# Kernel tuning notes

Hardware: AMD Instinct MI355X
Metric: run time of the kernel (lower is better)

Reference implementation:

```python
import jax, jax.numpy as jnp
import numpy as np

N_NODES = 500_000
MEM_DIM = 256
MSG_DIM = 256
N_UPD = 100_000


def setup_inputs() -> dict:
    key = jax.random.key(0)
    ks = jax.random.split(key, 10)
    s = 1.0 / np.sqrt(MEM_DIM)
    return {
        "unique_node_ids": jnp.arange(N_UPD, dtype=jnp.int64)
        if jax.config.jax_enable_x64 else jnp.arange(N_UPD, dtype=jnp.int32),
        "unique_messages": jax.random.normal(ks[0], (N_UPD, MSG_DIM), jnp.float32),
        "timestamps": jax.random.uniform(ks[1], (N_UPD,), jnp.float32),
        "net_transaction_amounts": jax.random.normal(ks[2], (N_UPD,), jnp.float32),
        "memory": jax.random.normal(ks[3], (N_NODES, MEM_DIM), jnp.float32),
        "last_update": jnp.zeros((N_NODES,), jnp.float32),
        "W_cat": jax.random.normal(ks[4], (MEM_DIM, MSG_DIM + 1), jnp.float32) * s,
        "b_cat": jnp.zeros((MEM_DIM,), jnp.float32),
        "W_ih": jax.random.normal(ks[5], (3 * MEM_DIM, MEM_DIM), jnp.float32) * s,
        "W_hh": jax.random.normal(ks[6], (3 * MEM_DIM, MEM_DIM), jnp.float32) * s,
        "b_ih": jnp.zeros((3 * MEM_DIM,), jnp.float32),
        "b_hh": jnp.zeros((3 * MEM_DIM,), jnp.float32),
    }


def _gru_cell(x, h, W_ih, W_hh, b_ih, b_hh):
    # torch.nn.GRUCell math
    gi = x @ W_ih.T + b_ih      # [N, 3*D]
    gh = h @ W_hh.T + b_hh      # [N, 3*D]
    i_r, i_z, i_n = jnp.split(gi, 3, axis=1)
    h_r, h_z, h_n = jnp.split(gh, 3, axis=1)
    r = jax.nn.sigmoid(i_r + h_r)
    z = jax.nn.sigmoid(i_z + h_z)
    n = jnp.tanh(i_n + r * h_n)
    return (1.0 - z) * n + z * h


def reference(unique_node_ids, unique_messages, timestamps, net_transaction_amounts,
              memory, last_update, W_cat, b_cat, W_ih, W_hh, b_ih, b_hh):
    # concat message with scalar amount, small linear projection
    cat = jnp.concatenate([unique_messages, net_transaction_amounts[:, None]], axis=1)
    final_inputs = cat @ W_cat.T + b_cat                # [N_upd, MEM_DIM]
    h = memory[unique_node_ids]                         # gather by id
    new_h = _gru_cell(final_inputs, h, W_ih, W_hh, b_ih, b_hh)
    updated_memory = memory.at[unique_node_ids].set(new_h)        # scatter back
    updated_last_update = last_update.at[unique_node_ids].set(timestamps)
    return updated_memory, updated_last_update
```

## Files before the change

kernel.cpp:

```cpp
#include <hip/hip_runtime.h>
#include <hip/hip_bf16.h>

typedef __attribute__((ext_vector_type(8))) short s16x8;
typedef __attribute__((ext_vector_type(4))) float f32x4;

__device__ __forceinline__ unsigned short f2bf(float x) {
    unsigned int u = __float_as_uint(x);
    u += 0x7fffu + ((u >> 16) & 1u);
    return (unsigned short)(u >> 16);
}
__device__ __forceinline__ float bf2f(unsigned short h) {
    return __uint_as_float((unsigned int)h << 16);
}
__device__ __forceinline__ s16x8 pack8(float4 a, float4 b) {
    return (s16x8){ (short)f2bf(a.x), (short)f2bf(a.y), (short)f2bf(a.z), (short)f2bf(a.w),
                    (short)f2bf(b.x), (short)f2bf(b.y), (short)f2bf(b.z), (short)f2bf(b.w) };
}
__device__ __forceinline__ void gload_lds16(const void* g, void* l) {
    __builtin_amdgcn_global_load_lds(
        (const __attribute__((address_space(1))) void*)g,
        (__attribute__((address_space(3))) void*)(unsigned int)(size_t)l,
        16, 0, 0);
}
__device__ __forceinline__ float sigf(float x) { return 1.f / (1.f + __expf(-x)); }
__device__ __forceinline__ float tanhfast(float x) {
    return 1.f - 2.f / (__expf(2.f * x) + 1.f);
}

__global__ void prep_w_kernel(const float* __restrict__ W_cat,
                              const float* __restrict__ b_cat,
                              const float* __restrict__ W_ih,
                              const float* __restrict__ W_hh,
                              const float* __restrict__ b_ih,
                              const int* __restrict__ ids,
                              unsigned short* __restrict__ wm,
                              unsigned short* __restrict__ whh,
                              float* __restrict__ wamt,
                              float* __restrict__ bcomb,
                              int* __restrict__ inv,
                              int M) {
    int idx = blockIdx.x * blockDim.x + threadIdx.x;
    const int NW = 768 * 256;
    if (idx < NW) {
        int g = idx >> 8, c = idx & 255;
        float s = 0.f;
        #pragma unroll 4
        for (int k = 0; k < 256; ++k) s += W_ih[g * 256 + k] * W_cat[k * 257 + c];
        wm[idx] = f2bf(s);
    } else if (idx < 2 * NW) {
        int t = idx - NW;
        whh[t] = f2bf(W_hh[t]);
    } else if (idx < 2 * NW + 768) {
        int g = idx - 2 * NW;
        float sa = 0.f, sb = 0.f;
        for (int k = 0; k < 256; ++k) {
            float w = W_ih[g * 256 + k];
            sa += w * W_cat[k * 257 + 256];
            sb += w * b_cat[k];
        }
        wamt[g] = sa;
        bcomb[g] = sb + b_ih[g];
    } else if (idx < 2 * NW + 768 + M) {
        int i = idx - (2 * NW + 768);
        inv[ids[i]] = i + 1;
    }
}

__device__ __forceinline__ void dma_w(const unsigned short* __restrict__ wm,
                                      const unsigned short* __restrict__ whh,
                                      int nc, int k0, char* swbuf, int tid) {
    #pragma unroll
    for (int it = 0; it < 6; ++it) {
        int q = tid + it * 512;
        int r = q >> 3;
        int part = (q & 7) ^ (r & 7);
        int pn = r >> 6, rr = r & 63;
        const unsigned short* src = (pn < 3)
            ? wm  + ((size_t)(pn * 256 + nc * 64 + rr)) * 256
            : whh + ((size_t)((pn - 3) * 256 + nc * 64 + rr)) * 256;
        gload_lds16((const char*)src + k0 * 2 + part * 16,
                    swbuf + (tid & ~63) * 16 + it * 8192);
    }
}

__global__ __launch_bounds__(512, 2)
void gru_kernel(const int* __restrict__ ids,
                const float* __restrict__ msgs,
                const float* __restrict__ memory,
                const unsigned short* __restrict__ wm,
                const unsigned short* __restrict__ whh,
                const float* __restrict__ wamt,
                const float* __restrict__ bcomb,
                const float* __restrict__ b_hh,
                const float* __restrict__ amt,
                float* __restrict__ out_mem,
                int M, int mtiles) {
    extern __shared__ char lds[];
    char* sm  = lds;
    char* sh  = lds + 16384;
    char* sw0 = lds + 32768;
    char* sw1 = lds + 81920;

    int g = blockIdx.x;
    int xcd = g & 7, s = g >> 3;
    int nc = s & 3;
    int mtile = (s >> 2) * 8 + xcd;
    if (mtile >= mtiles) return;
    int m0 = mtile * 128;

    int tid = threadIdx.x;
    int lane = tid & 63;
    int w = tid >> 6;
    int wr = w >> 2, wc = w & 3;

    int row0 = tid >> 3, row1 = (tid + 512) >> 3;
    int part = tid & 7;
    int gr0 = m0 + row0; if (gr0 >= M) gr0 = M - 1;
    int gr1 = m0 + row1; if (gr1 >= M) gr1 = M - 1;
    const float* mp0 = msgs + (size_t)gr0 * 256 + part * 8;
    const float* mp1 = msgs + (size_t)gr1 * 256 + part * 8;
    const float* hp0 = memory + (size_t)ids[gr0] * 256 + part * 8;
    const float* hp1 = memory + (size_t)ids[gr1] * 256 + part * 8;
    int ld0 = row0 * 128 + ((part ^ (row0 & 7)) * 16);
    int ld1 = row1 * 128 + ((part ^ (row1 & 7)) * 16);

    float4 ma0, mb0, ma1, mb1, ha0, hb0, ha1, hb1;
    {
        int k0 = ((nc + 1) & 3) * 64;
        ma0 = *(const float4*)(mp0 + k0);  mb0 = *(const float4*)(mp0 + k0 + 4);
        ma1 = *(const float4*)(mp1 + k0);  mb1 = *(const float4*)(mp1 + k0 + 4);
        ha0 = *(const float4*)(hp0 + k0);  hb0 = *(const float4*)(hp0 + k0 + 4);
        ha1 = *(const float4*)(hp1 + k0);  hb1 = *(const float4*)(hp1 + k0 + 4);
        dma_w(wm, whh, nc, k0, sw0, tid);
        *(s16x8*)(sm + ld0) = pack8(ma0, mb0);
        *(s16x8*)(sm + ld1) = pack8(ma1, mb1);
        *(s16x8*)(sh + ld0) = pack8(ha0, hb0);
        *(s16x8*)(sh + ld1) = pack8(ha1, hb1);
    }
    __syncthreads();

    f32x4 acc[6][4];
    #pragma unroll
    for (int pn = 0; pn < 6; ++pn)
        #pragma unroll
        for (int mf = 0; mf < 4; ++mf) acc[pn][mf] = (f32x4){0.f, 0.f, 0.f, 0.f};

    #pragma unroll
    for (int ks = 0; ks < 4; ++ks) {
        char* swc = (ks & 1) ? sw1 : sw0;
        if (ks < 3) {
            int k0 = ((nc + 2 + ks) & 3) * 64;
            ma0 = *(const float4*)(mp0 + k0);  mb0 = *(const float4*)(mp0 + k0 + 4);
            ma1 = *(const float4*)(mp1 + k0);  mb1 = *(const float4*)(mp1 + k0 + 4);
            ha0 = *(const float4*)(hp0 + k0);  hb0 = *(const float4*)(hp0 + k0 + 4);
            ha1 = *(const float4*)(hp1 + k0);  hb1 = *(const float4*)(hp1 + k0 + 4);
            dma_w(wm, whh, nc, k0, (ks & 1) ? sw0 : sw1, tid);
        }
        #pragma unroll
        for (int c = 0; c < 2; ++c) {
            int p = c * 4 + (lane >> 4);
            s16x8 ax[4], ah[4], bw[6];
            #pragma unroll
            for (int mf = 0; mf < 4; ++mf) {
                int row = wr * 64 + mf * 16 + (lane & 15);
                int off = row * 128 + ((p ^ (row & 7)) * 16);
                ax[mf] = *(const s16x8*)(sm + off);
                ah[mf] = *(const s16x8*)(sh + off);
            }
            #pragma unroll
            for (int pn = 0; pn < 6; ++pn) {
                int r = pn * 64 + wc * 16 + (lane & 15);
                bw[pn] = *(const s16x8*)(swc + r * 128 + ((p ^ (r & 7)) * 16));
            }
            #pragma unroll
            for (int pn = 0; pn < 6; ++pn)
                #pragma unroll
                for (int mf = 0; mf < 4; ++mf)
                    acc[pn][mf] = __builtin_amdgcn_mfma_f32_16x16x32_bf16(
                        (pn < 3) ? ax[mf] : ah[mf], bw[pn], acc[pn][mf], 0, 0, 0);
        }
        if (ks < 3) {
            __syncthreads();
            *(s16x8*)(sm + ld0) = pack8(ma0, mb0);
            *(s16x8*)(sm + ld1) = pack8(ma1, mb1);
            *(s16x8*)(sh + ld0) = pack8(ha0, hb0);
            *(s16x8*)(sh + ld1) = pack8(ha1, hb1);
            __syncthreads();
        }
    }

    int colL = wc * 16 + (lane & 15);
    int col = nc * 64 + colL;
    float bi0 = bcomb[col], bi1 = bcomb[256 + col], bi2 = bcomb[512 + col];
    float bh0 = b_hh[col],  bh1 = b_hh[256 + col],  bh2 = b_hh[512 + col];
    float wa0 = wamt[col],  wa1 = wamt[256 + col],  wa2 = wamt[512 + col];
    int hpart = colL >> 3, hbyte = (colL & 7) << 1;
    #pragma unroll
    for (int mf = 0; mf < 4; ++mf) {
        int rb = wr * 64 + mf * 16 + (lane >> 4) * 4;
        #pragma unroll
        for (int r = 0; r < 4; ++r) {
            int rl = rb + r;
            int grow = m0 + rl; if (grow >= M) grow = M - 1;
            int gid = ids[grow];
            float amtv = amt[grow];
            float hv = bf2f(*(const unsigned short*)(
                sh + rl * 128 + ((hpart ^ (rl & 7)) << 4) + hbyte));
            float ir = acc[0][mf][r] + bi0 + amtv * wa0;
            float iz = acc[1][mf][r] + bi1 + amtv * wa1;
            float in_ = acc[2][mf][r] + bi2 + amtv * wa2;
            float hr = acc[3][mf][r] + bh0;
            float hz = acc[4][mf][r] + bh1;
            float hn = acc[5][mf][r] + bh2;
            float rg = sigf(ir + hr);
            float zg = sigf(iz + hz);
            float ng = tanhfast(in_ + rg * hn);
            out_mem[(size_t)gid * 256 + col] = (1.f - zg) * ng + zg * hv;
        }
    }
}

__global__ __launch_bounds__(256)
void copy_kernel(const float* __restrict__ memory,
                 const int* __restrict__ inv,
                 const float* __restrict__ lu,
                 const float* __restrict__ ts,
                 float* __restrict__ out_mem,
                 float* __restrict__ out_lu,
                 int N) {
    int wid = (blockIdx.x * blockDim.x + threadIdx.x) >> 6;
    int lane = threadIdx.x & 63;
    int nw = (gridDim.x * blockDim.x) >> 6;
    for (int base = wid; base < N; base += nw * 4) {
        int  r0 = base, r1 = base + nw, r2 = base + 2 * nw, r3 = base + 3 * nw;
        bool d0 = (r0 < N) && (inv[r0] == 0);
        bool d1 = (r1 < N) && (inv[r1] == 0);
        bool d2 = (r2 < N) && (inv[r2] == 0);
        bool d3 = (r3 < N) && (inv[r3] == 0);
        float4 v0, v1, v2, v3;
        if (d0) v0 = ((const float4*)(memory + (size_t)r0 * 256))[lane];
        if (d1) v1 = ((const float4*)(memory + (size_t)r1 * 256))[lane];
        if (d2) v2 = ((const float4*)(memory + (size_t)r2 * 256))[lane];
        if (d3) v3 = ((const float4*)(memory + (size_t)r3 * 256))[lane];
        if (d0) ((float4*)(out_mem + (size_t)r0 * 256))[lane] = v0;
        if (d1) ((float4*)(out_mem + (size_t)r1 * 256))[lane] = v1;
        if (d2) ((float4*)(out_mem + (size_t)r2 * 256))[lane] = v2;
        if (d3) ((float4*)(out_mem + (size_t)r3 * 256))[lane] = v3;
    }
    int gidx = blockIdx.x * blockDim.x + threadIdx.x;
    int stride = gridDim.x * blockDim.x;
    for (int i = gidx; i < N; i += stride) {
        int iv = inv[i];
        out_lu[i] = iv ? ts[iv - 1] : lu[i];
    }
}

extern "C" void kernel_launch(void* const* d_in, const int* in_sizes, int n_in,
                              void* d_out, int out_size, void* d_ws, size_t ws_size,
                              hipStream_t stream) {
    const int*   ids   = (const int*)  d_in[0];
    const float* msgs  = (const float*)d_in[1];
    const float* ts    = (const float*)d_in[2];
    const float* amt   = (const float*)d_in[3];
    const float* mem   = (const float*)d_in[4];
    const float* lu    = (const float*)d_in[5];
    const float* W_cat = (const float*)d_in[6];
    const float* b_cat = (const float*)d_in[7];
    const float* W_ih  = (const float*)d_in[8];
    const float* W_hh  = (const float*)d_in[9];
    const float* b_ih  = (const float*)d_in[10];
    const float* b_hh  = (const float*)d_in[11];

    int M = in_sizes[0];
    int N = in_sizes[5];

    float* out_mem = (float*)d_out;
    float* out_lu  = out_mem + (size_t)N * 256;

    char* ws = (char*)d_ws;
    unsigned short* wm    = (unsigned short*)ws;
    unsigned short* whh   = wm + 768 * 256;
    float*          wamt  = (float*)(whh + 768 * 256);
    float*          bcomb = wamt + 768;
    int*            inv   = (int*)(bcomb + 768);

    (void)hipMemsetAsync(inv, 0, (size_t)N * 4, stream);

    int prep_items = 2 * 768 * 256 + 768 + M;
    prep_w_kernel<<<(prep_items + 255) / 256, 256, 0, stream>>>(
        W_cat, b_cat, W_ih, W_hh, b_ih, ids, wm, whh, wamt, bcomb, inv, M);

    int mtiles = (M + 127) / 128;
    int mt8 = ((mtiles + 7) / 8) * 8;
    (void)hipFuncSetAttribute((const void*)gru_kernel,
                              hipFuncAttributeMaxDynamicSharedMemorySize, 131072);
    gru_kernel<<<mt8 * 4, 512, 131072, stream>>>(
        ids, msgs, mem, wm, whh, wamt, bcomb, b_hh, amt, out_mem, M, mtiles);

    copy_kernel<<<2048, 256, 0, stream>>>(mem, inv, lu, ts, out_mem, out_lu, N);
}
```

Measured before the change: 396.7 us.

## Shrink GRU tiles to 64 rows, single-buffer weights, fold memset and lu scatter

```diff
diff --git a/kernel.cpp b/kernel.cpp
--- a/kernel.cpp
+++ b/kernel.cpp
@@ -38,7 +38,7 @@
                               float* __restrict__ wamt,
                               float* __restrict__ bcomb,
                               int* __restrict__ inv,
-                              int M) {
+                              int N, int M) {
     int idx = blockIdx.x * blockDim.x + threadIdx.x;
     const int NW = 768 * 256;
     if (idx < NW) {
@@ -60,163 +60,11 @@
         }
         wamt[g] = sa;
         bcomb[g] = sb + b_ih[g];
-    } else if (idx < 2 * NW + 768 + M) {
-        int i = idx - (2 * NW + 768);
+    } else if (idx < 2 * NW + 768 + N) {
+        inv[idx - (2 * NW + 768)] = 0;
+    } else if (idx < 2 * NW + 768 + N + M) {
+        int i = idx - (2 * NW + 768 + N);
         inv[ids[i]] = i + 1;
-    }
-}
-
-__device__ __forceinline__ void dma_w(const unsigned short* __restrict__ wm,
-                                      const unsigned short* __restrict__ whh,
-                                      int nc, int k0, char* swbuf, int tid) {
-    #pragma unroll
-    for (int it = 0; it < 6; ++it) {
-        int q = tid + it * 512;
-        int r = q >> 3;
-        int part = (q & 7) ^ (r & 7);
-        int pn = r >> 6, rr = r & 63;
-        const unsigned short* src = (pn < 3)
-            ? wm  + ((size_t)(pn * 256 + nc * 64 + rr)) * 256
-            : whh + ((size_t)((pn - 3) * 256 + nc * 64 + rr)) * 256;
-        gload_lds16((const char*)src + k0 * 2 + part * 16,
-                    swbuf + (tid & ~63) * 16 + it * 8192);
-    }
-}
-
-__global__ __launch_bounds__(512, 2)
-void gru_kernel(const int* __restrict__ ids,
-                const float* __restrict__ msgs,
-                const float* __restrict__ memory,
-                const unsigned short* __restrict__ wm,
-                const unsigned short* __restrict__ whh,
-                const float* __restrict__ wamt,
-                const float* __restrict__ bcomb,
-                const float* __restrict__ b_hh,
-                const float* __restrict__ amt,
-                float* __restrict__ out_mem,
-                int M, int mtiles) {
-    extern __shared__ char lds[];
-    char* sm  = lds;
-    char* sh  = lds + 16384;
-    char* sw0 = lds + 32768;
-    char* sw1 = lds + 81920;
-
-    int g = blockIdx.x;
-    int xcd = g & 7, s = g >> 3;
-    int nc = s & 3;
-    int mtile = (s >> 2) * 8 + xcd;
-    if (mtile >= mtiles) return;
-    int m0 = mtile * 128;
-
-    int tid = threadIdx.x;
-    int lane = tid & 63;
-    int w = tid >> 6;
-    int wr = w >> 2, wc = w & 3;
-
-    int row0 = tid >> 3, row1 = (tid + 512) >> 3;
-    int part = tid & 7;
-    int gr0 = m0 + row0; if (gr0 >= M) gr0 = M - 1;
-    int gr1 = m0 + row1; if (gr1 >= M) gr1 = M - 1;
-    const float* mp0 = msgs + (size_t)gr0 * 256 + part * 8;
-    const float* mp1 = msgs + (size_t)gr1 * 256 + part * 8;
-    const float* hp0 = memory + (size_t)ids[gr0] * 256 + part * 8;
-    const float* hp1 = memory + (size_t)ids[gr1] * 256 + part * 8;
-    int ld0 = row0 * 128 + ((part ^ (row0 & 7)) * 16);
-    int ld1 = row1 * 128 + ((part ^ (row1 & 7)) * 16);
-
-    float4 ma0, mb0, ma1, mb1, ha0, hb0, ha1, hb1;
-    {
-        int k0 = ((nc + 1) & 3) * 64;
-        ma0 = *(const float4*)(mp0 + k0);  mb0 = *(const float4*)(mp0 + k0 + 4);
-        ma1 = *(const float4*)(mp1 + k0);  mb1 = *(const float4*)(mp1 + k0 + 4);
-        ha0 = *(const float4*)(hp0 + k0);  hb0 = *(const float4*)(hp0 + k0 + 4);
-        ha1 = *(const float4*)(hp1 + k0);  hb1 = *(const float4*)(hp1 + k0 + 4);
-        dma_w(wm, whh, nc, k0, sw0, tid);
-        *(s16x8*)(sm + ld0) = pack8(ma0, mb0);
-        *(s16x8*)(sm + ld1) = pack8(ma1, mb1);
-        *(s16x8*)(sh + ld0) = pack8(ha0, hb0);
-        *(s16x8*)(sh + ld1) = pack8(ha1, hb1);
-    }
-    __syncthreads();
-
-    f32x4 acc[6][4];
-    #pragma unroll
-    for (int pn = 0; pn < 6; ++pn)
-        #pragma unroll
-        for (int mf = 0; mf < 4; ++mf) acc[pn][mf] = (f32x4){0.f, 0.f, 0.f, 0.f};
-
-    #pragma unroll
-    for (int ks = 0; ks < 4; ++ks) {
-        char* swc = (ks & 1) ? sw1 : sw0;
-        if (ks < 3) {
-            int k0 = ((nc + 2 + ks) & 3) * 64;
-            ma0 = *(const float4*)(mp0 + k0);  mb0 = *(const float4*)(mp0 + k0 + 4);
-            ma1 = *(const float4*)(mp1 + k0);  mb1 = *(const float4*)(mp1 + k0 + 4);
-            ha0 = *(const float4*)(hp0 + k0);  hb0 = *(const float4*)(hp0 + k0 + 4);
-            ha1 = *(const float4*)(hp1 + k0);  hb1 = *(const float4*)(hp1 + k0 + 4);
-            dma_w(wm, whh, nc, k0, (ks & 1) ? sw0 : sw1, tid);
-        }
-        #pragma unroll
-        for (int c = 0; c < 2; ++c) {
-            int p = c * 4 + (lane >> 4);
-            s16x8 ax[4], ah[4], bw[6];
-            #pragma unroll
-            for (int mf = 0; mf < 4; ++mf) {
-                int row = wr * 64 + mf * 16 + (lane & 15);
-                int off = row * 128 + ((p ^ (row & 7)) * 16);
-                ax[mf] = *(const s16x8*)(sm + off);
-                ah[mf] = *(const s16x8*)(sh + off);
-            }
-            #pragma unroll
-            for (int pn = 0; pn < 6; ++pn) {
-                int r = pn * 64 + wc * 16 + (lane & 15);
-                bw[pn] = *(const s16x8*)(swc + r * 128 + ((p ^ (r & 7)) * 16));
-            }
-            #pragma unroll
-            for (int pn = 0; pn < 6; ++pn)
-                #pragma unroll
-                for (int mf = 0; mf < 4; ++mf)
-                    acc[pn][mf] = __builtin_amdgcn_mfma_f32_16x16x32_bf16(
-                        (pn < 3) ? ax[mf] : ah[mf], bw[pn], acc[pn][mf], 0, 0, 0);
-        }
-        if (ks < 3) {
-            __syncthreads();
-            *(s16x8*)(sm + ld0) = pack8(ma0, mb0);
-            *(s16x8*)(sm + ld1) = pack8(ma1, mb1);
-            *(s16x8*)(sh + ld0) = pack8(ha0, hb0);
-            *(s16x8*)(sh + ld1) = pack8(ha1, hb1);
-            __syncthreads();
-        }
-    }
-
-    int colL = wc * 16 + (lane & 15);
-    int col = nc * 64 + colL;
-    float bi0 = bcomb[col], bi1 = bcomb[256 + col], bi2 = bcomb[512 + col];
-    float bh0 = b_hh[col],  bh1 = b_hh[256 + col],  bh2 = b_hh[512 + col];
-    float wa0 = wamt[col],  wa1 = wamt[256 + col],  wa2 = wamt[512 + col];
-    int hpart = colL >> 3, hbyte = (colL & 7) << 1;
-    #pragma unroll
-    for (int mf = 0; mf < 4; ++mf) {
-        int rb = wr * 64 + mf * 16 + (lane >> 4) * 4;
-        #pragma unroll
-        for (int r = 0; r < 4; ++r) {
-            int rl = rb + r;
-            int grow = m0 + rl; if (grow >= M) grow = M - 1;
-            int gid = ids[grow];
-            float amtv = amt[grow];
-            float hv = bf2f(*(const unsigned short*)(
-                sh + rl * 128 + ((hpart ^ (rl & 7)) << 4) + hbyte));
-            float ir = acc[0][mf][r] + bi0 + amtv * wa0;
-            float iz = acc[1][mf][r] + bi1 + amtv * wa1;
-            float in_ = acc[2][mf][r] + bi2 + amtv * wa2;
-            float hr = acc[3][mf][r] + bh0;
-            float hz = acc[4][mf][r] + bh1;
-            float hn = acc[5][mf][r] + bh2;
-            float rg = sigf(ir + hr);
-            float zg = sigf(iz + hz);
-            float ng = tanhfast(in_ + rg * hn);
-            out_mem[(size_t)gid * 256 + col] = (1.f - zg) * ng + zg * hv;
-        }
     }
 }
 
@@ -224,7 +72,6 @@
 void copy_kernel(const float* __restrict__ memory,
                  const int* __restrict__ inv,
                  const float* __restrict__ lu,
-                 const float* __restrict__ ts,
                  float* __restrict__ out_mem,
                  float* __restrict__ out_lu,
                  int N) {
@@ -249,9 +96,165 @@
     }
     int gidx = blockIdx.x * blockDim.x + threadIdx.x;
     int stride = gridDim.x * blockDim.x;
-    for (int i = gidx; i < N; i += stride) {
-        int iv = inv[i];
-        out_lu[i] = iv ? ts[iv - 1] : lu[i];
+    for (int i = gidx; i < N; i += stride) out_lu[i] = lu[i];
+}
+
+__device__ __forceinline__ void dma_w(const unsigned short* __restrict__ wm,
+                                      const unsigned short* __restrict__ whh,
+                                      int nc, int k0, char* swbuf, int tid) {
+    #pragma unroll
+    for (int it = 0; it < 12; ++it) {
+        int q = tid + it * 256;
+        int r = q >> 3;
+        int part = (q & 7) ^ (r & 7);
+        int pn = r >> 6, rr = r & 63;
+        const unsigned short* src = (pn < 3)
+            ? wm  + ((size_t)(pn * 256 + nc * 64 + rr)) * 256
+            : whh + ((size_t)((pn - 3) * 256 + nc * 64 + rr)) * 256;
+        gload_lds16((const char*)src + k0 * 2 + part * 16,
+                    swbuf + (q & ~63) * 16);
+    }
+}
+
+__global__ __launch_bounds__(256, 2)
+void gru_kernel(const int* __restrict__ ids,
+                const float* __restrict__ msgs,
+                const float* __restrict__ memory,
+                const unsigned short* __restrict__ wm,
+                const unsigned short* __restrict__ whh,
+                const float* __restrict__ wamt,
+                const float* __restrict__ bcomb,
+                const float* __restrict__ b_hh,
+                const float* __restrict__ amt,
+                const float* __restrict__ ts,
+                float* __restrict__ out_mem,
+                float* __restrict__ out_lu,
+                int M, int mtiles) {
+    extern __shared__ char lds[];
+    char* sm = lds;
+    char* sh = lds + 8192;
+    char* sw = lds + 16384;
+
+    int g = blockIdx.x;
+    int xcd = g & 7, s = g >> 3;
+    int nc = s & 3;
+    int mtile = (s >> 2) * 8 + xcd;
+    if (mtile >= mtiles) return;
+    int m0 = mtile * 64;
+
+    int tid = threadIdx.x;
+    int lane = tid & 63;
+    int wc = tid >> 6;
+
+    int row0 = tid >> 3, row1 = (tid + 256) >> 3;
+    int part = tid & 7;
+    int gr0 = m0 + row0; if (gr0 >= M) gr0 = M - 1;
+    int gr1 = m0 + row1; if (gr1 >= M) gr1 = M - 1;
+    const float* mp0 = msgs + (size_t)gr0 * 256 + part * 8;
+    const float* mp1 = msgs + (size_t)gr1 * 256 + part * 8;
+    const float* hp0 = memory + (size_t)ids[gr0] * 256 + part * 8;
+    const float* hp1 = memory + (size_t)ids[gr1] * 256 + part * 8;
+    int ld0 = row0 * 128 + ((part ^ (row0 & 7)) * 16);
+    int ld1 = row1 * 128 + ((part ^ (row1 & 7)) * 16);
+
+    s16x8 pm0, pm1, ph0, ph1;
+    {
+        int k0 = ((nc + 1) & 3) * 64;
+        float4 a0 = *(const float4*)(mp0 + k0), b0 = *(const float4*)(mp0 + k0 + 4);
+        float4 a1 = *(const float4*)(mp1 + k0), b1 = *(const float4*)(mp1 + k0 + 4);
+        float4 c0 = *(const float4*)(hp0 + k0), d0 = *(const float4*)(hp0 + k0 + 4);
+        float4 c1 = *(const float4*)(hp1 + k0), d1 = *(const float4*)(hp1 + k0 + 4);
+        dma_w(wm, whh, nc, k0, sw, tid);
+        *(s16x8*)(sm + ld0) = pack8(a0, b0);
+        *(s16x8*)(sm + ld1) = pack8(a1, b1);
+        *(s16x8*)(sh + ld0) = pack8(c0, d0);
+        *(s16x8*)(sh + ld1) = pack8(c1, d1);
+    }
+    __syncthreads();
+
+    f32x4 acc[6][4];
+    #pragma unroll
+    for (int pn = 0; pn < 6; ++pn)
+        #pragma unroll
+        for (int mf = 0; mf < 4; ++mf) acc[pn][mf] = (f32x4){0.f, 0.f, 0.f, 0.f};
+
+    #pragma unroll
+    for (int ks = 0; ks < 4; ++ks) {
+        float4 a0, b0, a1, b1, c0, d0, c1, d1;
+        if (ks < 3) {
+            int k0 = ((nc + 2 + ks) & 3) * 64;
+            a0 = *(const float4*)(mp0 + k0);  b0 = *(const float4*)(mp0 + k0 + 4);
+            a1 = *(const float4*)(mp1 + k0);  b1 = *(const float4*)(mp1 + k0 + 4);
+            c0 = *(const float4*)(hp0 + k0);  d0 = *(const float4*)(hp0 + k0 + 4);
+            c1 = *(const float4*)(hp1 + k0);  d1 = *(const float4*)(hp1 + k0 + 4);
+        }
+        #pragma unroll
+        for (int c = 0; c < 2; ++c) {
+            int p = c * 4 + (lane >> 4);
+            s16x8 ax[4], ah[4], bw[6];
+            #pragma unroll
+            for (int mf = 0; mf < 4; ++mf) {
+                int row = mf * 16 + (lane & 15);
+                int off = row * 128 + ((p ^ (row & 7)) * 16);
+                ax[mf] = *(const s16x8*)(sm + off);
+                ah[mf] = *(const s16x8*)(sh + off);
+            }
+            #pragma unroll
+            for (int pn = 0; pn < 6; ++pn) {
+                int r = pn * 64 + wc * 16 + (lane & 15);
+                bw[pn] = *(const s16x8*)(sw + r * 128 + ((p ^ (r & 7)) * 16));
+            }
+            #pragma unroll
+            for (int pn = 0; pn < 6; ++pn)
+                #pragma unroll
+                for (int mf = 0; mf < 4; ++mf)
+                    acc[pn][mf] = __builtin_amdgcn_mfma_f32_16x16x32_bf16(
+                        (pn < 3) ? ax[mf] : ah[mf], bw[pn], acc[pn][mf], 0, 0, 0);
+        }
+        if (ks < 3) {
+            pm0 = pack8(a0, b0); pm1 = pack8(a1, b1);
+            ph0 = pack8(c0, d0); ph1 = pack8(c1, d1);
+            __syncthreads();
+            int k0 = ((nc + 2 + ks) & 3) * 64;
+            dma_w(wm, whh, nc, k0, sw, tid);
+            *(s16x8*)(sm + ld0) = pm0;
+            *(s16x8*)(sm + ld1) = pm1;
+            *(s16x8*)(sh + ld0) = ph0;
+            *(s16x8*)(sh + ld1) = ph1;
+            __syncthreads();
+        }
+    }
+
+    int colL = wc * 16 + (lane & 15);
+    int col = nc * 64 + colL;
+    float bi0 = bcomb[col], bi1 = bcomb[256 + col], bi2 = bcomb[512 + col];
+    float bh0 = b_hh[col],  bh1 = b_hh[256 + col],  bh2 = b_hh[512 + col];
+    float wa0 = wamt[col],  wa1 = wamt[256 + col],  wa2 = wamt[512 + col];
+    int hpart = colL >> 3, hbyte = (colL & 7) << 1;
+    bool lu_thread = (nc == 0) && ((lane & 15) == 0) && (wc == 0);
+    #pragma unroll
+    for (int mf = 0; mf < 4; ++mf) {
+        int rb = mf * 16 + (lane >> 4) * 4;
+        #pragma unroll
+        for (int r = 0; r < 4; ++r) {
+            int rl = rb + r;
+            int grow = m0 + rl; if (grow >= M) grow = M - 1;
+            int gid = ids[grow];
+            float amtv = amt[grow];
+            float hv = bf2f(*(const unsigned short*)(
+                sh + rl * 128 + ((hpart ^ (rl & 7)) << 4) + hbyte));
+            float ir = acc[0][mf][r] + bi0 + amtv * wa0;
+            float iz = acc[1][mf][r] + bi1 + amtv * wa1;
+            float in_ = acc[2][mf][r] + bi2 + amtv * wa2;
+            float hr = acc[3][mf][r] + bh0;
+            float hz = acc[4][mf][r] + bh1;
+            float hn = acc[5][mf][r] + bh2;
+            float rg = sigf(ir + hr);
+            float zg = sigf(iz + hz);
+            float ng = tanhfast(in_ + rg * hn);
+            out_mem[(size_t)gid * 256 + col] = (1.f - zg) * ng + zg * hv;
+            if (lu_thread) out_lu[gid] = ts[grow];
+        }
     }
 }
 
@@ -284,18 +287,17 @@
     float*          bcomb = wamt + 768;
     int*            inv   = (int*)(bcomb + 768);
 
-    (void)hipMemsetAsync(inv, 0, (size_t)N * 4, stream);
-
-    int prep_items = 2 * 768 * 256 + 768 + M;
+    int prep_items = 2 * 768 * 256 + 768 + N + M;
     prep_w_kernel<<<(prep_items + 255) / 256, 256, 0, stream>>>(
-        W_cat, b_cat, W_ih, W_hh, b_ih, ids, wm, whh, wamt, bcomb, inv, M);
-
-    int mtiles = (M + 127) / 128;
+        W_cat, b_cat, W_ih, W_hh, b_ih, ids, wm, whh, wamt, bcomb, inv, N, M);
+
+    copy_kernel<<<2048, 256, 0, stream>>>(mem, inv, lu, out_mem, out_lu, N);
+
+    int mtiles = (M + 63) / 64;
     int mt8 = ((mtiles + 7) / 8) * 8;
     (void)hipFuncSetAttribute((const void*)gru_kernel,
-                              hipFuncAttributeMaxDynamicSharedMemorySize, 131072);
-    gru_kernel<<<mt8 * 4, 512, 131072, stream>>>(
-        ids, msgs, mem, wm, whh, wamt, bcomb, b_hh, amt, out_mem, M, mtiles);
-
-    copy_kernel<<<2048, 256, 0, stream>>>(mem, inv, lu, ts, out_mem, out_lu, N);
-}
+                              hipFuncAttributeMaxDynamicSharedMemorySize, 65536);
+    gru_kernel<<<mt8 * 4, 256, 65536, stream>>>(
+        ids, msgs, mem, wm, whh, wamt, bcomb, b_hh, amt, ts,
+        out_mem, out_lu, M, mtiles);
+}
```

New measurement: 425.2 us. +7.2%, slower.
